# Kernel optimization log

Hardware: AMD Instinct MI355X
Metric: run time of the kernel (lower is better)

The kernel has to match this reference:

```python
import jax, jax.numpy as jnp
import numpy as np
import itertools

# ---- model dimensions ----
NELEC = 10   # total electrons
NSPIN = 2    # spin_split = 2 -> equal split (5, 5)
NPER = 5     # electrons per spin block
D = 3        # spatial dimension
NION = 2     # number of ions (diatomic)
DP = 32      # backflow output feature dim d'
NDENSE = 64  # ndense_resnet


def _perms_and_signs(n):
    perms = np.array(list(itertools.permutations(range(n))), dtype=np.int32)
    signs = np.empty(len(perms), dtype=np.float32)
    for i, p in enumerate(perms):
        inv = sum(1 for a in range(n) for b in range(a + 1, n) if p[a] > p[b])
        signs[i] = -1.0 if inv % 2 else 1.0
    return jnp.asarray(perms), jnp.asarray(signs)

# constant permutation indices/signs (closed over; not differentiated)
PERMS, SIGNS = _perms_and_signs(NPER)  # (120, 5), (120,)


def setup_inputs() -> dict:
    key = jax.random.key(0)
    ks = jax.random.split(key, 8)
    B = 2048
    feat = NION * D + NION  # backflow input features per electron: r_ei flat + |r_ei|
    nin = NPER * DP         # flattened spin-block input to each ResNet
    return {
        "elec_pos": jax.random.normal(ks[0], (B, NELEC, D), jnp.float32),
        "ion_pos": jax.random.normal(ks[1], (NION, D), jnp.float32) * 2.0,
        "bf_w": jax.random.normal(ks[2], (feat, DP), jnp.float32) / np.sqrt(feat),
        "bf_b": jnp.zeros((DP,), jnp.float32),
        "w0": jax.random.normal(ks[3], (NSPIN, nin, NDENSE), jnp.float32) / np.sqrt(nin),
        "b0": jnp.zeros((NSPIN, NDENSE), jnp.float32),
        "w1": jax.random.normal(ks[4], (NSPIN, NDENSE, NDENSE), jnp.float32) / np.sqrt(NDENSE),
        "b1": jnp.zeros((NSPIN, NDENSE), jnp.float32),
        "w2": jax.random.normal(ks[5], (NSPIN, NDENSE, 1), jnp.float32) / np.sqrt(NDENSE),
        "b2": jnp.zeros((NSPIN, 1), jnp.float32),
        "jastrow_kernel": jnp.ones((NION,), jnp.float32),
    }


def _spin_antisym(block, W0, B0, W1, B1, W2, B2):
    # block: (B, NPER, DP) one spin block of the 1e stream
    B = block.shape[0]
    xp = block[:, PERMS, :]                  # (B, nperm, NPER, DP) all permutations
    xp = xp.reshape(B, PERMS.shape[0], NPER * DP)
    # SimpleResNet: dense->act, residual middle layer, final linear to 1
    h = jnp.tanh(xp @ W0 + B0)
    h = jnp.tanh(h @ W1 + B1) + h            # residual (shapes match)
    out = (h @ W2 + B2)[..., 0]              # (B, nperm)
    return jnp.sum(out * SIGNS, axis=-1)     # signed perm-sum -> (B,)


def reference(elec_pos, ion_pos, bf_w, bf_b, w0, b0, w1, b1, w2, b2, jastrow_kernel):
    B = elec_pos.shape[0]
    # backflow: r_ei features -> dense -> tanh
    r_ei = elec_pos[..., :, None, :] - ion_pos          # (B, nelec, nion, d)
    r_norm = jnp.linalg.norm(r_ei, axis=-1)             # (B, nelec, nion)
    feats = jnp.concatenate([r_ei.reshape(B, NELEC, NION * D), r_norm], axis=-1)
    stream_1e = jnp.tanh(feats @ bf_w + bf_b)           # (B, nelec, DP)
    # split into equal spin blocks (spin_split=2)
    blocks = jnp.stack(jnp.split(stream_1e, NSPIN, axis=-2), axis=0)  # (NSPIN, B, NPER, DP)
    per_spin = jax.vmap(_spin_antisym)(blocks, w0, b0, w1, b1, w2, b2)  # (NSPIN, B)
    antisymmetric_part = jnp.log(jnp.abs(jnp.prod(per_spin, axis=0)))   # (B,)
    # isotropic atomic exponential decay jastrow (log domain)
    jastrow_part = -jnp.sum(jastrow_kernel * r_norm, axis=(-1, -2))     # (B,)
    return antisymmetric_part + jastrow_part
```

## Files before the change

### kernel.cpp

```cpp
#include <hip/hip_runtime.h>
#include <math.h>

#define NELEC 10
#define NSPIN 2
#define NPER 5
#define DIM 3
#define NION 2
#define DP 32
#define NDENSE 64
#define NPERM 120
#define RS 324
#define HTS 124

#define POOL_WORDS (NDENSE * HTS)

typedef float v2f __attribute__((ext_vector_type(2)));
typedef float v4f __attribute__((ext_vector_type(4)));

#define PK_FMA_LO(acc, hp, wp) \
    asm("v_pk_fma_f32 %0, %1, %2, %0 op_sel_hi:[1,0,1]" : "+v"(acc) : "v"(hp), "v"(wp))
#define PK_FMA_HI(acc, hp, wp) \
    asm("v_pk_fma_f32 %0, %1, %2, %0 op_sel:[0,1,0] op_sel_hi:[1,1,1]" : "+v"(acc) : "v"(hp), "v"(wp))

__device__ __forceinline__ float fast_tanh(float x) {
    float e = __expf(2.0f * x);
    return 1.0f - 2.0f * __builtin_amdgcn_rcpf(e + 1.0f);
}

__device__ __forceinline__ unsigned pick_remove(unsigned& el, int d) {
    unsigned v = (el >> (4 * d)) & 0xFu;
    unsigned low = el & ((1u << (4 * d)) - 1u);
    el = low | ((el >> (4 * (d + 1))) << (4 * d));
    return v;
}

__global__ __launch_bounds__(256, 1) void antisym_fused(
    const float* __restrict__ elec_pos, const float* __restrict__ ion_pos,
    const float* __restrict__ bf_w, const float* __restrict__ bf_b,
    const float* __restrict__ w0, const float* __restrict__ b0,
    const float* __restrict__ w1, const float* __restrict__ b1,
    const float* __restrict__ w2, const float* __restrict__ jk,
    float* __restrict__ out, int B)
{
    const int b = blockIdx.x;
    const int t = threadIdx.x;
    const int s = t >> 7;
    const int ts = t & 127;
    const int wave = (t >> 6) & 1;
    const int lane = t & 63;

    __shared__ __align__(16) float pool[NSPIN][POOL_WORDS];
    __shared__ double red_h[NSPIN][2];
    __shared__ double red_j[NSPIN][2];
    __shared__ float jterm[2 * NELEC];

    float* s1e = pool[s];
    #define GROW(j) (pool[s] + 160 + (j) * RS)
    #define HTROW(k) (pool[s] + (k) * HTS)

    const float* ep = elec_pos + (b * NELEC + s * NPER) * DIM;
    const float i0x = ion_pos[0], i0y = ion_pos[1], i0z = ion_pos[2];
    const float i1x = ion_pos[3], i1y = ion_pos[4], i1z = ion_pos[5];
    for (int idx = ts; idx < NPER * DP; idx += 128) {
        int j = idx >> 5, c = idx & 31;
        float ex = ep[j * 3 + 0], ey = ep[j * 3 + 1], ez = ep[j * 3 + 2];
        float dx0 = ex - i0x, dy0 = ey - i0y, dz0 = ez - i0z;
        float dx1 = ex - i1x, dy1 = ey - i1y, dz1 = ez - i1z;
        float n0 = sqrtf(dx0 * dx0 + dy0 * dy0 + dz0 * dz0);
        float n1 = sqrtf(dx1 * dx1 + dy1 * dy1 + dz1 * dz1);
        float acc = bf_b[c];
        acc += dx0 * bf_w[0 * DP + c];
        acc += dy0 * bf_w[1 * DP + c];
        acc += dz0 * bf_w[2 * DP + c];
        acc += dx1 * bf_w[3 * DP + c];
        acc += dy1 * bf_w[4 * DP + c];
        acc += dz1 * bf_w[5 * DP + c];
        acc += n0 * bf_w[6 * DP + c];
        acc += n1 * bf_w[7 * DP + c];
        s1e[idx] = fast_tanh(acc);
    }
    if (t < 2 * NELEC) {
        int e = t >> 1, ion = t & 1;
        const float* epb = elec_pos + b * NELEC * DIM;
        float ex = epb[e * 3 + 0], ey = epb[e * 3 + 1], ez = epb[e * 3 + 2];
        float ix = ion_pos[ion * 3 + 0], iy = ion_pos[ion * 3 + 1], iz = ion_pos[ion * 3 + 2];
        float dx = ex - ix, dy = ey - iy, dz = ez - iz;
        jterm[t] = jk[ion] * sqrtf(dx * dx + dy * dy + dz * dz);
    }
    __syncthreads();

    const float* w0s = w0 + s * (NPER * DP) * NDENSE;
    #pragma unroll
    for (int m = 0; m < 3; m++) {
        const int i = wave + 2 * m;
        if (i < NPER) {
            float wcol[DP];
            #pragma unroll
            for (int k = 0; k < DP; k++) wcol[k] = w0s[(i * DP + k) * NDENSE + lane];
            #pragma unroll
            for (int j = 0; j < NPER; j++) {
                float acc = 0.f;
                #pragma unroll
                for (int q = 0; q < 8; q++) {
                    float4 sv = *(const float4*)(s1e + j * DP + q * 4);
                    acc += sv.x * wcol[q * 4 + 0];
                    acc += sv.y * wcol[q * 4 + 1];
                    acc += sv.z * wcol[q * 4 + 2];
                    acc += sv.w * wcol[q * 4 + 3];
                }
                GROW(j)[i * NDENSE + lane] = acc;
            }
        }
    }
    __syncthreads();

    const float* b0s = b0 + s * NDENSE;
    const float* w2s = w2 + s * NDENSE;

    const int pid = wave * 60 + lane;
    float sign = 0.f;
    int p0 = 0, p1 = 0, p2 = 0, p3 = 0, p4 = 0;
    if (lane < 60) {
        int p = pid;
        unsigned el = 0x43210u;
        int d0 = p / 24; p -= d0 * 24;
        int d1 = p / 6;  p -= d1 * 6;
        int d2 = p / 2;  p -= d2 * 2;
        int d3 = p;
        p0 = pick_remove(el, d0);
        p1 = pick_remove(el, d1);
        p2 = pick_remove(el, d2);
        p3 = pick_remove(el, d3);
        p4 = el & 0xF;
        sign = ((d0 + d1 + d2 + d3) & 1) ? -1.f : 1.f;
    }
    const float* g0 = GROW(p0) + 0 * NDENSE;
    const float* g1 = GROW(p1) + 1 * NDENSE;
    const float* g2 = GROW(p2) + 2 * NDENSE;
    const float* g3 = GROW(p3) + 3 * NDENSE;
    const float* g4 = GROW(p4) + 4 * NDENSE;

    float h[NDENSE];
    float hdot = 0.f;
    #pragma unroll
    for (int cc = 0; cc < NDENSE / 4; cc++) {
        float4 a = *(const float4*)(b0s + cc * 4);
        float4 q;
        q = *(const float4*)(g0 + cc * 4); a.x += q.x; a.y += q.y; a.z += q.z; a.w += q.w;
        q = *(const float4*)(g1 + cc * 4); a.x += q.x; a.y += q.y; a.z += q.z; a.w += q.w;
        q = *(const float4*)(g2 + cc * 4); a.x += q.x; a.y += q.y; a.z += q.z; a.w += q.w;
        q = *(const float4*)(g3 + cc * 4); a.x += q.x; a.y += q.y; a.z += q.z; a.w += q.w;
        q = *(const float4*)(g4 + cc * 4); a.x += q.x; a.y += q.y; a.z += q.z; a.w += q.w;
        float t0 = fast_tanh(a.x), t1 = fast_tanh(a.y), t2 = fast_tanh(a.z), t3 = fast_tanh(a.w);
        h[cc * 4 + 0] = t0; h[cc * 4 + 1] = t1; h[cc * 4 + 2] = t2; h[cc * 4 + 3] = t3;
        hdot += t0 * w2s[cc * 4 + 0] + t1 * w2s[cc * 4 + 1]
              + t2 * w2s[cc * 4 + 2] + t3 * w2s[cc * 4 + 3];
    }

    double dvh = (double)(sign * hdot);
    #pragma unroll
    for (int off = 32; off > 0; off >>= 1) dvh += __shfl_down(dvh, off, 64);
    if (lane == 0) red_h[s][wave] = dvh;

    __syncthreads();

    if (lane < 60) {
        #pragma unroll
        for (int k = 0; k < NDENSE; k++) HTROW(k)[pid] = h[k];
    }
    __syncthreads();

    const int pg = lane >> 3, jg = lane & 7;
    const int pb = wave ? (56 + 8 * pg) : (8 * pg);
    const float* w1s = w1 + s * NDENSE * NDENSE;
    const float* b1s = b1 + s * NDENSE;
    const float* wgp = w1s + 8 * jg;

    v2f vp[4][8];
    #pragma unroll
    for (int ip = 0; ip < 4; ip++)
        #pragma unroll
        for (int r = 0; r < 8; r++) vp[ip][r] = (v2f)(0.f);

    v4f ha_n = *(const v4f*)(&HTROW(0)[pb]);
    v4f hb_n = *(const v4f*)(&HTROW(0)[pb + 4]);
    v4f wa_n = *(const v4f*)(wgp);
    v4f wb_n = *(const v4f*)(wgp + 4);
    #pragma unroll 4
    for (int k = 0; k < NDENSE; k++) {
        const v4f ha = ha_n, hb = hb_n, wa = wa_n, wb = wb_n;
        if (k + 1 < NDENSE) {
            ha_n = *(const v4f*)(&HTROW(k + 1)[pb]);
            hb_n = *(const v4f*)(&HTROW(k + 1)[pb + 4]);
            wa_n = *(const v4f*)(wgp + (k + 1) * NDENSE);
            wb_n = *(const v4f*)(wgp + (k + 1) * NDENSE + 4);
        }
        v2f hp[4] = {ha.xy, ha.zw, hb.xy, hb.zw};
        v2f wp[4] = {wa.xy, wa.zw, wb.xy, wb.zw};
        #pragma unroll
        for (int ip = 0; ip < 4; ip++) {
            PK_FMA_LO(vp[ip][0], hp[ip], wp[0]);
            PK_FMA_HI(vp[ip][1], hp[ip], wp[0]);
            PK_FMA_LO(vp[ip][2], hp[ip], wp[1]);
            PK_FMA_HI(vp[ip][3], hp[ip], wp[1]);
            PK_FMA_LO(vp[ip][4], hp[ip], wp[2]);
            PK_FMA_HI(vp[ip][5], hp[ip], wp[2]);
            PK_FMA_LO(vp[ip][6], hp[ip], wp[3]);
            PK_FMA_HI(vp[ip][7], hp[ip], wp[3]);
        }
    }

    float4 b1a = *(const float4*)(b1s + 8 * jg);
    float4 b1b = *(const float4*)(b1s + 8 * jg + 4);
    float4 w2a = *(const float4*)(w2s + 8 * jg);
    float4 w2b = *(const float4*)(w2s + 8 * jg + 4);
    const float b1v[8] = {b1a.x, b1a.y, b1a.z, b1a.w, b1b.x, b1b.y, b1b.z, b1b.w};
    const float w2v[8] = {w2a.x, w2a.y, w2a.z, w2a.w, w2b.x, w2b.y, w2b.z, w2b.w};

    float lanesum = 0.f;
    #pragma unroll
    for (int i = 0; i < 8; i++) {
        int p = pb + i;
        int d0 = p / 24;  int r0 = p - 24 * d0;
        int d1 = r0 / 6;  int r1 = r0 - 6 * d1;
        int d2 = r1 >> 1; int d3 = r1 & 1;
        float sgn = ((d0 + d1 + d2 + d3) & 1) ? -1.f : 1.f;
        if (wave == 1 && pg == 0) sgn = 0.f;
        float si = 0.f;
        #pragma unroll
        for (int r = 0; r < 8; r++) {
            float vir = (i & 1) ? vp[i >> 1][r].y : vp[i >> 1][r].x;
            si = fmaf(fast_tanh(vir + b1v[r]), w2v[r], si);
        }
        lanesum = fmaf(sgn, si, lanesum);
    }

    double dvj = (double)lanesum;
    #pragma unroll
    for (int off = 32; off > 0; off >>= 1) dvj += __shfl_down(dvj, off, 64);
    if (lane == 0) red_j[s][wave] = dvj;
    __syncthreads();

    if (t == 0) {
        float ps0 = (float)((red_h[0][0] + red_h[0][1]) + (red_j[0][0] + red_j[0][1]));
        float ps1 = (float)((red_h[1][0] + red_h[1][1]) + (red_j[1][0] + red_j[1][1]));
        float jas = 0.f;
        #pragma unroll
        for (int i = 0; i < 2 * NELEC; i++) jas += jterm[i];
        out[b] = logf(fabsf(ps0 * ps1)) - jas;
    }
}

extern "C" void kernel_launch(void* const* d_in, const int* in_sizes, int n_in,
                              void* d_out, int out_size, void* d_ws, size_t ws_size,
                              hipStream_t stream) {
    const float* elec_pos = (const float*)d_in[0];
    const float* ion_pos  = (const float*)d_in[1];
    const float* bf_w     = (const float*)d_in[2];
    const float* bf_b     = (const float*)d_in[3];
    const float* w0       = (const float*)d_in[4];
    const float* b0       = (const float*)d_in[5];
    const float* w1       = (const float*)d_in[6];
    const float* b1       = (const float*)d_in[7];
    const float* w2       = (const float*)d_in[8];
    const float* jk       = (const float*)d_in[10];
    float* out = (float*)d_out;

    const int B = in_sizes[0] / (NELEC * DIM);

    hipLaunchKernelGGL(antisym_fused,
                       dim3(B), dim3(256), 0, stream,
                       elec_pos, ion_pos, bf_w, bf_b, w0, b0, w1, b1, w2, jk, out, B);
}
```

Before: 155.6 us.

## Interleave first-layer tanh with second-layer GEMM in K-chunks to cut registers and LDS

```diff
diff --git a/kernel.cpp b/kernel.cpp
--- a/kernel.cpp
+++ b/kernel.cpp
@@ -11,8 +11,9 @@
 #define NPERM 120
 #define RS 324
 #define HTS 124
-
-#define POOL_WORDS (NDENSE * HTS)
+#define KQ 16
+
+#define POOL_WORDS (160 + NPER * RS + KQ * HTS)
 
 typedef float v2f __attribute__((ext_vector_type(2)));
 typedef float v4f __attribute__((ext_vector_type(4)));
@@ -34,7 +35,7 @@
     return v;
 }
 
-__global__ __launch_bounds__(256, 1) void antisym_fused(
+__global__ __launch_bounds__(256, 4) void antisym_fused(
     const float* __restrict__ elec_pos, const float* __restrict__ ion_pos,
     const float* __restrict__ bf_w, const float* __restrict__ bf_b,
     const float* __restrict__ w0, const float* __restrict__ b0,
@@ -55,8 +56,8 @@
     __shared__ float jterm[2 * NELEC];
 
     float* s1e = pool[s];
-    #define GROW(j) (pool[s] + 160 + (j) * RS)
-    #define HTROW(k) (pool[s] + (k) * HTS)
+    #define GROW(j)   (pool[s] + 160 + (j) * RS)
+    #define HTQROW(k) (pool[s] + 160 + NPER * RS + (k) * HTS)
 
     const float* ep = elec_pos + (b * NELEC + s * NPER) * DIM;
     const float i0x = ion_pos[0], i0y = ion_pos[1], i0z = ion_pos[2];
@@ -116,6 +117,8 @@
 
     const float* b0s = b0 + s * NDENSE;
     const float* w2s = w2 + s * NDENSE;
+    const float* b1s = b1 + s * NDENSE;
+    const float* w1s = w1 + s * NDENSE * NDENSE;
 
     const int pid = wave * 60 + lane;
     float sign = 0.f;
@@ -140,75 +143,76 @@
     const float* g3 = GROW(p3) + 3 * NDENSE;
     const float* g4 = GROW(p4) + 4 * NDENSE;
 
-    float h[NDENSE];
+    const int pg = lane >> 3, jg = lane & 7;
+    const int pb = wave ? (56 + 8 * pg) : (8 * pg);
+    const float* wgp = w1s + 8 * jg;
+
+    v2f vp[4][8];
+    #pragma unroll
+    for (int ip = 0; ip < 4; ip++)
+        #pragma unroll
+        for (int r = 0; r < 8; r++) vp[ip][r] = (v2f)(0.f);
+
     float hdot = 0.f;
-    #pragma unroll
-    for (int cc = 0; cc < NDENSE / 4; cc++) {
-        float4 a = *(const float4*)(b0s + cc * 4);
-        float4 q;
-        q = *(const float4*)(g0 + cc * 4); a.x += q.x; a.y += q.y; a.z += q.z; a.w += q.w;
-        q = *(const float4*)(g1 + cc * 4); a.x += q.x; a.y += q.y; a.z += q.z; a.w += q.w;
-        q = *(const float4*)(g2 + cc * 4); a.x += q.x; a.y += q.y; a.z += q.z; a.w += q.w;
-        q = *(const float4*)(g3 + cc * 4); a.x += q.x; a.y += q.y; a.z += q.z; a.w += q.w;
-        q = *(const float4*)(g4 + cc * 4); a.x += q.x; a.y += q.y; a.z += q.z; a.w += q.w;
-        float t0 = fast_tanh(a.x), t1 = fast_tanh(a.y), t2 = fast_tanh(a.z), t3 = fast_tanh(a.w);
-        h[cc * 4 + 0] = t0; h[cc * 4 + 1] = t1; h[cc * 4 + 2] = t2; h[cc * 4 + 3] = t3;
-        hdot += t0 * w2s[cc * 4 + 0] + t1 * w2s[cc * 4 + 1]
-              + t2 * w2s[cc * 4 + 2] + t3 * w2s[cc * 4 + 3];
+
+    for (int qq = 0; qq < 4; qq++) {
+        float hq[KQ];
+        #pragma unroll
+        for (int c = 0; c < 4; c++) {
+            const int cc = qq * 4 + c;
+            float4 a = *(const float4*)(b0s + cc * 4);
+            float4 q;
+            q = *(const float4*)(g0 + cc * 4); a.x += q.x; a.y += q.y; a.z += q.z; a.w += q.w;
+            q = *(const float4*)(g1 + cc * 4); a.x += q.x; a.y += q.y; a.z += q.z; a.w += q.w;
+            q = *(const float4*)(g2 + cc * 4); a.x += q.x; a.y += q.y; a.z += q.z; a.w += q.w;
+            q = *(const float4*)(g3 + cc * 4); a.x += q.x; a.y += q.y; a.z += q.z; a.w += q.w;
+            q = *(const float4*)(g4 + cc * 4); a.x += q.x; a.y += q.y; a.z += q.z; a.w += q.w;
+            float t0 = fast_tanh(a.x), t1 = fast_tanh(a.y), t2 = fast_tanh(a.z), t3 = fast_tanh(a.w);
+            hq[c * 4 + 0] = t0; hq[c * 4 + 1] = t1; hq[c * 4 + 2] = t2; hq[c * 4 + 3] = t3;
+            hdot += t0 * w2s[cc * 4 + 0] + t1 * w2s[cc * 4 + 1]
+                  + t2 * w2s[cc * 4 + 2] + t3 * w2s[cc * 4 + 3];
+        }
+
+        if (lane < 60) {
+            #pragma unroll
+            for (int kk = 0; kk < KQ; kk++) HTQROW(kk)[pid] = hq[kk];
+        }
+        __syncthreads();
+
+        v4f ha_n = *(const v4f*)(&HTQROW(0)[pb]);
+        v4f hb_n = *(const v4f*)(&HTQROW(0)[pb + 4]);
+        v4f wa_n = *(const v4f*)(wgp + (qq * KQ) * NDENSE);
+        v4f wb_n = *(const v4f*)(wgp + (qq * KQ) * NDENSE + 4);
+        #pragma unroll 4
+        for (int kk = 0; kk < KQ; kk++) {
+            const v4f ha = ha_n, hb = hb_n, wa = wa_n, wb = wb_n;
+            if (kk + 1 < KQ) {
+                ha_n = *(const v4f*)(&HTQROW(kk + 1)[pb]);
+                hb_n = *(const v4f*)(&HTQROW(kk + 1)[pb + 4]);
+                wa_n = *(const v4f*)(wgp + (qq * KQ + kk + 1) * NDENSE);
+                wb_n = *(const v4f*)(wgp + (qq * KQ + kk + 1) * NDENSE + 4);
+            }
+            v2f hp[4] = {ha.xy, ha.zw, hb.xy, hb.zw};
+            v2f wp[4] = {wa.xy, wa.zw, wb.xy, wb.zw};
+            #pragma unroll
+            for (int ip = 0; ip < 4; ip++) {
+                PK_FMA_LO(vp[ip][0], hp[ip], wp[0]);
+                PK_FMA_HI(vp[ip][1], hp[ip], wp[0]);
+                PK_FMA_LO(vp[ip][2], hp[ip], wp[1]);
+                PK_FMA_HI(vp[ip][3], hp[ip], wp[1]);
+                PK_FMA_LO(vp[ip][4], hp[ip], wp[2]);
+                PK_FMA_HI(vp[ip][5], hp[ip], wp[2]);
+                PK_FMA_LO(vp[ip][6], hp[ip], wp[3]);
+                PK_FMA_HI(vp[ip][7], hp[ip], wp[3]);
+            }
+        }
+        __syncthreads();
     }
 
     double dvh = (double)(sign * hdot);
     #pragma unroll
     for (int off = 32; off > 0; off >>= 1) dvh += __shfl_down(dvh, off, 64);
     if (lane == 0) red_h[s][wave] = dvh;
-
-    __syncthreads();
-
-    if (lane < 60) {
-        #pragma unroll
-        for (int k = 0; k < NDENSE; k++) HTROW(k)[pid] = h[k];
-    }
-    __syncthreads();
-
-    const int pg = lane >> 3, jg = lane & 7;
-    const int pb = wave ? (56 + 8 * pg) : (8 * pg);
-    const float* w1s = w1 + s * NDENSE * NDENSE;
-    const float* b1s = b1 + s * NDENSE;
-    const float* wgp = w1s + 8 * jg;
-
-    v2f vp[4][8];
-    #pragma unroll
-    for (int ip = 0; ip < 4; ip++)
-        #pragma unroll
-        for (int r = 0; r < 8; r++) vp[ip][r] = (v2f)(0.f);
-
-    v4f ha_n = *(const v4f*)(&HTROW(0)[pb]);
-    v4f hb_n = *(const v4f*)(&HTROW(0)[pb + 4]);
-    v4f wa_n = *(const v4f*)(wgp);
-    v4f wb_n = *(const v4f*)(wgp + 4);
-    #pragma unroll 4
-    for (int k = 0; k < NDENSE; k++) {
-        const v4f ha = ha_n, hb = hb_n, wa = wa_n, wb = wb_n;
-        if (k + 1 < NDENSE) {
-            ha_n = *(const v4f*)(&HTROW(k + 1)[pb]);
-            hb_n = *(const v4f*)(&HTROW(k + 1)[pb + 4]);
-            wa_n = *(const v4f*)(wgp + (k + 1) * NDENSE);
-            wb_n = *(const v4f*)(wgp + (k + 1) * NDENSE + 4);
-        }
-        v2f hp[4] = {ha.xy, ha.zw, hb.xy, hb.zw};
-        v2f wp[4] = {wa.xy, wa.zw, wb.xy, wb.zw};
-        #pragma unroll
-        for (int ip = 0; ip < 4; ip++) {
-            PK_FMA_LO(vp[ip][0], hp[ip], wp[0]);
-            PK_FMA_HI(vp[ip][1], hp[ip], wp[0]);
-            PK_FMA_LO(vp[ip][2], hp[ip], wp[1]);
-            PK_FMA_HI(vp[ip][3], hp[ip], wp[1]);
-            PK_FMA_LO(vp[ip][4], hp[ip], wp[2]);
-            PK_FMA_HI(vp[ip][5], hp[ip], wp[2]);
-            PK_FMA_LO(vp[ip][6], hp[ip], wp[3]);
-            PK_FMA_HI(vp[ip][7], hp[ip], wp[3]);
-        }
-    }
 
     float4 b1a = *(const float4*)(b1s + 8 * jg);
     float4 b1b = *(const float4*)(b1s + 8 * jg + 4);
```

After: 251.1 us. 1.61x slower.

## Split per-spin work into separate 128-thread blocks with combine kernel

Applied to the files above, without the earlier changes.

```diff
diff --git a/kernel.cpp b/kernel.cpp
--- a/kernel.cpp
+++ b/kernel.cpp
@@ -34,34 +34,34 @@
     return v;
 }
 
-__global__ __launch_bounds__(256, 1) void antisym_fused(
+__global__ __launch_bounds__(128, 1) __attribute__((amdgpu_num_vgpr(128)))
+void antisym_spin(
     const float* __restrict__ elec_pos, const float* __restrict__ ion_pos,
     const float* __restrict__ bf_w, const float* __restrict__ bf_b,
     const float* __restrict__ w0, const float* __restrict__ b0,
     const float* __restrict__ w1, const float* __restrict__ b1,
     const float* __restrict__ w2, const float* __restrict__ jk,
-    float* __restrict__ out, int B)
+    float* __restrict__ ws, int B)
 {
-    const int b = blockIdx.x;
+    const int b = blockIdx.x >> 1;
+    const int s = blockIdx.x & 1;
     const int t = threadIdx.x;
-    const int s = t >> 7;
-    const int ts = t & 127;
-    const int wave = (t >> 6) & 1;
+    const int wave = t >> 6;
     const int lane = t & 63;
 
-    __shared__ __align__(16) float pool[NSPIN][POOL_WORDS];
-    __shared__ double red_h[NSPIN][2];
-    __shared__ double red_j[NSPIN][2];
-    __shared__ float jterm[2 * NELEC];
-
-    float* s1e = pool[s];
-    #define GROW(j) (pool[s] + 160 + (j) * RS)
-    #define HTROW(k) (pool[s] + (k) * HTS)
+    __shared__ __align__(16) float pool[POOL_WORDS];
+    __shared__ double red_h[2];
+    __shared__ double red_j[2];
+    __shared__ float jterm[2 * NPER];
+
+    float* s1e = pool;
+    #define GROW(j)  (pool + 160 + (j) * RS)
+    #define HTROW(k) (pool + (k) * HTS)
 
     const float* ep = elec_pos + (b * NELEC + s * NPER) * DIM;
     const float i0x = ion_pos[0], i0y = ion_pos[1], i0z = ion_pos[2];
     const float i1x = ion_pos[3], i1y = ion_pos[4], i1z = ion_pos[5];
-    for (int idx = ts; idx < NPER * DP; idx += 128) {
+    for (int idx = t; idx < NPER * DP; idx += 128) {
         int j = idx >> 5, c = idx & 31;
         float ex = ep[j * 3 + 0], ey = ep[j * 3 + 1], ez = ep[j * 3 + 2];
         float dx0 = ex - i0x, dy0 = ey - i0y, dz0 = ez - i0z;
@@ -79,8 +79,8 @@
         acc += n1 * bf_w[7 * DP + c];
         s1e[idx] = fast_tanh(acc);
     }
-    if (t < 2 * NELEC) {
-        int e = t >> 1, ion = t & 1;
+    if (t < 2 * NPER) {
+        int e = s * NPER + (t >> 1), ion = t & 1;
         const float* epb = elec_pos + b * NELEC * DIM;
         float ex = epb[e * 3 + 0], ey = epb[e * 3 + 1], ez = epb[e * 3 + 2];
         float ix = ion_pos[ion * 3 + 0], iy = ion_pos[ion * 3 + 1], iz = ion_pos[ion * 3 + 2];
@@ -160,7 +160,7 @@
     double dvh = (double)(sign * hdot);
     #pragma unroll
     for (int off = 32; off > 0; off >>= 1) dvh += __shfl_down(dvh, off, 64);
-    if (lane == 0) red_h[s][wave] = dvh;
+    if (lane == 0) red_h[wave] = dvh;
 
     __syncthreads();
 
@@ -238,15 +238,27 @@
     double dvj = (double)lanesum;
     #pragma unroll
     for (int off = 32; off > 0; off >>= 1) dvj += __shfl_down(dvj, off, 64);
-    if (lane == 0) red_j[s][wave] = dvj;
+    if (lane == 0) red_j[wave] = dvj;
     __syncthreads();
 
     if (t == 0) {
-        float ps0 = (float)((red_h[0][0] + red_h[0][1]) + (red_j[0][0] + red_j[0][1]));
-        float ps1 = (float)((red_h[1][0] + red_h[1][1]) + (red_j[1][0] + red_j[1][1]));
+        float ps = (float)((red_h[0] + red_h[1]) + (red_j[0] + red_j[1]));
         float jas = 0.f;
         #pragma unroll
-        for (int i = 0; i < 2 * NELEC; i++) jas += jterm[i];
+        for (int i = 0; i < 2 * NPER; i++) jas += jterm[i];
+        ws[s * B + b] = ps;
+        ws[2 * B + s * B + b] = jas;
+    }
+}
+
+__global__ __launch_bounds__(256) void antisym_combine(
+    const float* __restrict__ ws, float* __restrict__ out, int B)
+{
+    int b = blockIdx.x * blockDim.x + threadIdx.x;
+    if (b < B) {
+        float ps0 = ws[b];
+        float ps1 = ws[B + b];
+        float jas = ws[2 * B + b] + ws[3 * B + b];
         out[b] = logf(fabsf(ps0 * ps1)) - jas;
     }
 }
@@ -265,10 +277,14 @@
     const float* w2       = (const float*)d_in[8];
     const float* jk       = (const float*)d_in[10];
     float* out = (float*)d_out;
+    float* ws  = (float*)d_ws;
 
     const int B = in_sizes[0] / (NELEC * DIM);
 
-    hipLaunchKernelGGL(antisym_fused,
-                       dim3(B), dim3(256), 0, stream,
-                       elec_pos, ion_pos, bf_w, bf_b, w0, b0, w1, b1, w2, jk, out, B);
-}
+    hipLaunchKernelGGL(antisym_spin,
+                       dim3(2 * B), dim3(128), 0, stream,
+                       elec_pos, ion_pos, bf_w, bf_b, w0, b0, w1, b1, w2, jk, ws, B);
+    hipLaunchKernelGGL(antisym_combine,
+                       dim3((B + 255) / 256), dim3(256), 0, stream,
+                       ws, out, B);
+}
```

Result: slower. 159.6 us (+2.6%).

## Move residual layer GEMM to MFMA f16 with split-precision hi/lo operands

Applied to the files above, without the earlier changes.

```diff
diff --git a/kernel.cpp b/kernel.cpp
--- a/kernel.cpp
+++ b/kernel.cpp
@@ -10,17 +10,17 @@
 #define NDENSE 64
 #define NPERM 120
 #define RS 324
-#define HTS 124
-
-#define POOL_WORDS (NDENSE * HTS)
-
-typedef float v2f __attribute__((ext_vector_type(2)));
-typedef float v4f __attribute__((ext_vector_type(4)));
-
-#define PK_FMA_LO(acc, hp, wp) \
-    asm("v_pk_fma_f32 %0, %1, %2, %0 op_sel_hi:[1,0,1]" : "+v"(acc) : "v"(hp), "v"(wp))
-#define PK_FMA_HI(acc, hp, wp) \
-    asm("v_pk_fma_f32 %0, %1, %2, %0 op_sel:[0,1,0] op_sel_hi:[1,1,1]" : "+v"(acc) : "v"(hp), "v"(wp))
+
+#define B1OFF 0
+#define W2OFF 64
+#define OVL 128
+#define GOFF (OVL + 160)
+#define PSTR 2560
+#define PROW 20
+#define POOL_WORDS (OVL + 2 * PSTR)
+
+typedef _Float16 f16x8 __attribute__((ext_vector_type(8)));
+typedef float f32x4 __attribute__((ext_vector_type(4)));
 
 __device__ __forceinline__ float fast_tanh(float x) {
     float e = __expf(2.0f * x);
@@ -34,12 +34,34 @@
     return v;
 }
 
+__device__ __forceinline__ float perm_sign(int p) {
+    int d0 = p / 24; int r0 = p - 24 * d0;
+    int d1 = r0 / 6; int r1 = r0 - 6 * d1;
+    int d2 = r1 >> 1; int d3 = r1 & 1;
+    return ((d0 + d1 + d2 + d3) & 1) ? -1.f : 1.f;
+}
+
+__global__ __launch_bounds__(256) void prep_w1(const float* __restrict__ w1,
+                                               _Float16* __restrict__ wsp)
+{
+    int idx = blockIdx.x * 256 + threadIdx.x;
+    if (idx < NSPIN * NDENSE * NDENSE) {
+        int s = idx >> 12; int r = idx & 4095; int k = r >> 6; int j = r & 63;
+        float x = w1[s * 4096 + k * 64 + j];
+        _Float16 hi = (_Float16)x;
+        float rem = x - (float)hi;
+        _Float16 lo = (_Float16)rem;
+        wsp[((0 * NSPIN + s) * 64 + j) * 64 + k] = hi;
+        wsp[((1 * NSPIN + s) * 64 + j) * 64 + k] = lo;
+    }
+}
+
 __global__ __launch_bounds__(256, 1) void antisym_fused(
     const float* __restrict__ elec_pos, const float* __restrict__ ion_pos,
     const float* __restrict__ bf_w, const float* __restrict__ bf_b,
     const float* __restrict__ w0, const float* __restrict__ b0,
-    const float* __restrict__ w1, const float* __restrict__ b1,
-    const float* __restrict__ w2, const float* __restrict__ jk,
+    const float* __restrict__ b1, const float* __restrict__ w2,
+    const float* __restrict__ jk, const _Float16* __restrict__ wsp,
     float* __restrict__ out, int B)
 {
     const int b = blockIdx.x;
@@ -50,13 +72,16 @@
     const int lane = t & 63;
 
     __shared__ __align__(16) float pool[NSPIN][POOL_WORDS];
+    __shared__ float signT[128];
     __shared__ double red_h[NSPIN][2];
     __shared__ double red_j[NSPIN][2];
     __shared__ float jterm[2 * NELEC];
 
-    float* s1e = pool[s];
-    #define GROW(j) (pool[s] + 160 + (j) * RS)
-    #define HTROW(k) (pool[s] + (k) * HTS)
+    float* b1L = pool[s] + B1OFF;
+    float* w2L = pool[s] + W2OFF;
+    float* s1e = pool[s] + OVL;
+    #define GROW(j) (pool[s] + GOFF + (j) * RS)
+    #define PARKP(sp) (pool[s] + OVL + (sp) * PSTR)
 
     const float* ep = elec_pos + (b * NELEC + s * NPER) * DIM;
     const float i0x = ion_pos[0], i0y = ion_pos[1], i0z = ion_pos[2];
@@ -79,6 +104,11 @@
         acc += n1 * bf_w[7 * DP + c];
         s1e[idx] = fast_tanh(acc);
     }
+    if (ts < NDENSE) {
+        b1L[ts] = b1[s * NDENSE + ts];
+        w2L[ts] = w2[s * NDENSE + ts];
+    }
+    if (t < 128) signT[t] = (t < NPERM) ? perm_sign(t) : 0.f;
     if (t < 2 * NELEC) {
         int e = t >> 1, ion = t & 1;
         const float* epb = elec_pos + b * NELEC * DIM;
@@ -140,7 +170,7 @@
     const float* g3 = GROW(p3) + 3 * NDENSE;
     const float* g4 = GROW(p4) + 4 * NDENSE;
 
-    float h[NDENSE];
+    f16x8 pkA[8], pkB[8];
     float hdot = 0.f;
     #pragma unroll
     for (int cc = 0; cc < NDENSE / 4; cc++) {
@@ -152,9 +182,15 @@
         q = *(const float4*)(g3 + cc * 4); a.x += q.x; a.y += q.y; a.z += q.z; a.w += q.w;
         q = *(const float4*)(g4 + cc * 4); a.x += q.x; a.y += q.y; a.z += q.z; a.w += q.w;
         float t0 = fast_tanh(a.x), t1 = fast_tanh(a.y), t2 = fast_tanh(a.z), t3 = fast_tanh(a.w);
-        h[cc * 4 + 0] = t0; h[cc * 4 + 1] = t1; h[cc * 4 + 2] = t2; h[cc * 4 + 3] = t3;
         hdot += t0 * w2s[cc * 4 + 0] + t1 * w2s[cc * 4 + 1]
               + t2 * w2s[cc * 4 + 2] + t3 * w2s[cc * 4 + 3];
+        const int vi = (cc >> 3) * 4 + ((cc & 7) >> 1);
+        const int po = 4 * (cc & 1);
+        _Float16 h_; float r_;
+        h_ = (_Float16)t0; r_ = t0 - (float)h_; pkA[vi][po + 0] = h_; pkB[vi][po + 0] = (_Float16)r_;
+        h_ = (_Float16)t1; r_ = t1 - (float)h_; pkA[vi][po + 1] = h_; pkB[vi][po + 1] = (_Float16)r_;
+        h_ = (_Float16)t2; r_ = t2 - (float)h_; pkA[vi][po + 2] = h_; pkB[vi][po + 2] = (_Float16)r_;
+        h_ = (_Float16)t3; r_ = t3 - (float)h_; pkA[vi][po + 3] = h_; pkB[vi][po + 3] = (_Float16)r_;
     }
 
     double dvh = (double)(sign * hdot);
@@ -162,77 +198,71 @@
     for (int off = 32; off > 0; off >>= 1) dvh += __shfl_down(dvh, off, 64);
     if (lane == 0) red_h[s][wave] = dvh;
 
-    __syncthreads();
-
-    if (lane < 60) {
-        #pragma unroll
-        for (int k = 0; k < NDENSE; k++) HTROW(k)[pid] = h[k];
-    }
-    __syncthreads();
-
-    const int pg = lane >> 3, jg = lane & 7;
-    const int pb = wave ? (56 + 8 * pg) : (8 * pg);
-    const float* w1s = w1 + s * NDENSE * NDENSE;
-    const float* b1s = b1 + s * NDENSE;
-    const float* wgp = w1s + 8 * jg;
-
-    v2f vp[4][8];
-    #pragma unroll
-    for (int ip = 0; ip < 4; ip++)
-        #pragma unroll
-        for (int r = 0; r < 8; r++) vp[ip][r] = (v2f)(0.f);
-
-    v4f ha_n = *(const v4f*)(&HTROW(0)[pb]);
-    v4f hb_n = *(const v4f*)(&HTROW(0)[pb + 4]);
-    v4f wa_n = *(const v4f*)(wgp);
-    v4f wb_n = *(const v4f*)(wgp + 4);
-    #pragma unroll 4
-    for (int k = 0; k < NDENSE; k++) {
-        const v4f ha = ha_n, hb = hb_n, wa = wa_n, wb = wb_n;
-        if (k + 1 < NDENSE) {
-            ha_n = *(const v4f*)(&HTROW(k + 1)[pb]);
-            hb_n = *(const v4f*)(&HTROW(k + 1)[pb + 4]);
-            wa_n = *(const v4f*)(wgp + (k + 1) * NDENSE);
-            wb_n = *(const v4f*)(wgp + (k + 1) * NDENSE + 4);
-        }
-        v2f hp[4] = {ha.xy, ha.zw, hb.xy, hb.zw};
-        v2f wp[4] = {wa.xy, wa.zw, wb.xy, wb.zw};
-        #pragma unroll
-        for (int ip = 0; ip < 4; ip++) {
-            PK_FMA_LO(vp[ip][0], hp[ip], wp[0]);
-            PK_FMA_HI(vp[ip][1], hp[ip], wp[0]);
-            PK_FMA_LO(vp[ip][2], hp[ip], wp[1]);
-            PK_FMA_HI(vp[ip][3], hp[ip], wp[1]);
-            PK_FMA_LO(vp[ip][4], hp[ip], wp[2]);
-            PK_FMA_HI(vp[ip][5], hp[ip], wp[2]);
-            PK_FMA_LO(vp[ip][6], hp[ip], wp[3]);
-            PK_FMA_HI(vp[ip][7], hp[ip], wp[3]);
-        }
-    }
-
-    float4 b1a = *(const float4*)(b1s + 8 * jg);
-    float4 b1b = *(const float4*)(b1s + 8 * jg + 4);
-    float4 w2a = *(const float4*)(w2s + 8 * jg);
-    float4 w2b = *(const float4*)(w2s + 8 * jg + 4);
-    const float b1v[8] = {b1a.x, b1a.y, b1a.z, b1a.w, b1b.x, b1b.y, b1b.z, b1b.w};
-    const float w2v[8] = {w2a.x, w2a.y, w2a.z, w2a.w, w2b.x, w2b.y, w2b.z, w2b.w};
-
+    const int lg = lane >> 4, lr = lane & 15;
+    const int prow = (lane < 60) ? pid : (120 + wave * 4 + (lane - 60));
+
+    f16x8 zf;
+    #pragma unroll
+    for (int e = 0; e < 8; e++) zf[e] = (_Float16)0.f;
+
+    f32x4 acc[4][4];
+    #pragma unroll
+    for (int mt = 0; mt < 4; mt++)
+        #pragma unroll
+        for (int nt = 0; nt < 4; nt++)
+            #pragma unroll
+            for (int e = 0; e < 4; e++) acc[mt][nt][e] = 0.f;
+
+    #pragma unroll
+    for (int ch = 0; ch < 2; ch++) {
+        __syncthreads();
+        #pragma unroll
+        for (int c = 0; c < 4; c++) {
+            *(f16x8*)(PARKP(0) + prow * PROW + c * 4) = (lane < 60) ? pkA[ch * 4 + c] : zf;
+            *(f16x8*)(PARKP(1) + prow * PROW + c * 4) = (lane < 60) ? pkB[ch * 4 + c] : zf;
+        }
+        __syncthreads();
+
+        f16x8 Ba[4], Bb[4];
+        #pragma unroll
+        for (int nt = 0; nt < 4; nt++) {
+            Ba[nt] = *(const f16x8*)(wsp + ((0 * NSPIN + s) * 64 + nt * 16 + lr) * 64 + ch * 32 + lg * 8);
+            Bb[nt] = *(const f16x8*)(wsp + ((1 * NSPIN + s) * 64 + nt * 16 + lr) * 64 + ch * 32 + lg * 8);
+        }
+        #pragma unroll
+        for (int mt = 0; mt < 4; mt++) {
+            const float* ar = PARKP(0) + (wave * 64 + mt * 16 + lr) * PROW + lg * 4;
+            f16x8 Aa = *(const f16x8*)ar;
+            f16x8 Ab = *(const f16x8*)(ar + PSTR);
+            #pragma unroll
+            for (int nt = 0; nt < 4; nt++) {
+                acc[mt][nt] = __builtin_amdgcn_mfma_f32_16x16x32_f16(Ab, Bb[nt], acc[mt][nt], 0, 0, 0);
+                acc[mt][nt] = __builtin_amdgcn_mfma_f32_16x16x32_f16(Ab, Ba[nt], acc[mt][nt], 0, 0, 0);
+                acc[mt][nt] = __builtin_amdgcn_mfma_f32_16x16x32_f16(Aa, Bb[nt], acc[mt][nt], 0, 0, 0);
+                acc[mt][nt] = __builtin_amdgcn_mfma_f32_16x16x32_f16(Aa, Ba[nt], acc[mt][nt], 0, 0, 0);
+            }
+        }
+    }
+
+    float bv[4], wv[4];
+    #pragma unroll
+    for (int nt = 0; nt < 4; nt++) {
+        bv[nt] = b1L[nt * 16 + lr];
+        wv[nt] = w2L[nt * 16 + lr];
+    }
     float lanesum = 0.f;
     #pragma unroll
-    for (int i = 0; i < 8; i++) {
-        int p = pb + i;
-        int d0 = p / 24;  int r0 = p - 24 * d0;
-        int d1 = r0 / 6;  int r1 = r0 - 6 * d1;
-        int d2 = r1 >> 1; int d3 = r1 & 1;
-        float sgn = ((d0 + d1 + d2 + d3) & 1) ? -1.f : 1.f;
-        if (wave == 1 && pg == 0) sgn = 0.f;
-        float si = 0.f;
-        #pragma unroll
-        for (int r = 0; r < 8; r++) {
-            float vir = (i & 1) ? vp[i >> 1][r].y : vp[i >> 1][r].x;
-            si = fmaf(fast_tanh(vir + b1v[r]), w2v[r], si);
-        }
-        lanesum = fmaf(sgn, si, lanesum);
+    for (int mt = 0; mt < 4; mt++) {
+        #pragma unroll
+        for (int qr = 0; qr < 4; qr++) {
+            const int p = wave * 64 + mt * 16 + lg * 4 + qr;
+            float sgn = signT[p];
+            float si = 0.f;
+            #pragma unroll
+            for (int nt = 0; nt < 4; nt++)
+                si = fmaf(fast_tanh(acc[mt][nt][qr] + bv[nt]), wv[nt], si);
+            lanesum = fmaf(sgn, si, lanesum);
+        }
     }
 
     double dvj = (double)lanesum;
@@ -265,10 +295,12 @@
     const float* w2       = (const float*)d_in[8];
     const float* jk       = (const float*)d_in[10];
     float* out = (float*)d_out;
+    _Float16* wsp = (_Float16*)d_ws;
 
     const int B = in_sizes[0] / (NELEC * DIM);
 
+    hipLaunchKernelGGL(prep_w1, dim3(32), dim3(256), 0, stream, w1, wsp);
     hipLaunchKernelGGL(antisym_fused,
                        dim3(B), dim3(256), 0, stream,
-                       elec_pos, ion_pos, bf_w, bf_b, w0, b0, w1, b1, w2, jk, out, B);
-}
+                       elec_pos, ion_pos, bf_w, bf_b, w0, b0, b1, w2, jk, wsp, out, B);
+}
```

New measurement: 172.3 us. 1.11x slower.
